# Kernel optimization log

Measured on AMD Instinct MI355X. Metric: run time of the kernel, lower is better.

The kernel has to match this reference:

```python
import jax, jax.numpy as jnp
import numpy as np

KH, KW = 3, 3
STRIDE = 1
OUT_C = 512


def im2col(x, kh, kw, stride):
    # x: [N, C, H, W] -> col: [C*kh*kw, N*oh*ow]  (row order: C major, then kh, kw)
    N, C, H, W = x.shape
    oh = (H - kh) // stride + 1
    ow = (W - kw) // stride + 1
    rows = jnp.arange(oh)[:, None] * stride + jnp.arange(kh)[None, :]  # [oh, kh]
    cols = jnp.arange(ow)[:, None] * stride + jnp.arange(kw)[None, :]  # [ow, kw]
    # gather windows: result [N, C, oh, kh, ow, kw]
    A = x[:, :, rows[:, :, None, None], cols[None, None, :, :]]
    # permute to (C, kh, kw, N, oh, ow) then flatten, matching torch permute(1,4,5,0,2,3)
    col = jnp.transpose(A, (1, 3, 5, 0, 2, 4)).reshape(C * kh * kw, N * oh * ow)
    return col, oh, ow


def setup_inputs() -> dict:
    key = jax.random.key(0)
    k1, k2, k3 = jax.random.split(key, 3)
    N, C, H, W = 16, 256, 32, 32
    K_sel = (C * KH * KW) // 2  # 1152 rows kept by the binary mask
    x = jax.random.normal(k1, (N, C, H, W), dtype=jnp.float32)
    weight = jax.random.normal(k2, (K_sel, OUT_C), dtype=jnp.float32) * 0.02
    idx = jnp.sort(jax.random.randint(k3, (K_sel,), 0, C * KH * KW, dtype=jnp.int32))
    return {"x": x, "weight": weight, "idx": idx}


def reference(x, weight, idx):
    N = x.shape[0]
    col, oh, ow = im2col(x, KH, KW, STRIDE)          # [C*kh*kw, N*oh*ow]
    x_tile = col[idx, :].T                            # gather masked rows -> [N*oh*ow, K_sel]
    conv_out = x_tile @ weight                        # [N*oh*ow, out_c]
    conv_out = conv_out.reshape(N, oh * ow, OUT_C)
    conv_out = jnp.transpose(conv_out, (0, 2, 1)).reshape(N, OUT_C, oh, ow)
    return conv_out
```

## Files before the change

### kernel.cpp

```cpp
#include <hip/hip_runtime.h>
#include <stdint.h>

#define N_IMG   16
#define C_IN    256
#define H_IN    32
#define W_IN    32
#define OH      30
#define OW      30
#define K_SEL   1152
#define OUTC    512
#define RY_TOT  (N_IMG * OH)
#define M_HAT   (RY_TOT * 32)
#define X_ELEMS (N_IMG * C_IN * H_IN * W_IN)
#define OUT_SP  (OH * OW)
#define CHW     (C_IN * H_IN * W_IN)

#define TO      128
#define TM      64
#define NMT     (M_HAT / TM)
#define NOT     (OUTC / TO)
#define BSTR    40
#define KITER   (K_SEL / 32)

typedef float f32x4  __attribute__((ext_vector_type(4)));
typedef short bf16x8 __attribute__((ext_vector_type(8)));

__device__ __forceinline__ unsigned short f2bf(float f) {
    unsigned int u = __float_as_uint(f);
    u += 0x7FFFu + ((u >> 16) & 1u);
    return (unsigned short)(u >> 16);
}

__device__ __forceinline__ void gl_lds16(const void* g, void* lds) {
    __builtin_amdgcn_global_load_lds(
        (const __attribute__((address_space(1))) unsigned int*)g,
        (__attribute__((address_space(3))) unsigned int*)lds,
        16, 0, 0);
}

__global__ void prep_kernel(const int* __restrict__ idx, const float* __restrict__ w,
                            int* __restrict__ koff, unsigned short* __restrict__ wT) {
    __shared__ float tile[32][33];
    const int bx = blockIdx.x, by = blockIdx.y, t = threadIdx.x;

    if (by == 0) {
        int k = bx * 256 + t;
        if (k < K_SEL) {
            int v = idx[k];
            int c = v / 9, rem = v - c * 9;
            int i = rem / 3, j = rem - i * 3;
            koff[k] = c * (H_IN * W_IN) + i * W_IN + j;
        }
    }
    const int s0 = bx * 32, o0 = by * 32;
    const int oc = t & 31, sg = t >> 5;
#pragma unroll
    for (int i = 0; i < 4; ++i) {
        int sl = sg * 4 + i;
        tile[sl][oc] = w[(s0 + sl) * OUTC + o0 + oc];
    }
    __syncthreads();
    const int ol = t >> 3, sq = t & 7;
    unsigned int u0 = (unsigned int)f2bf(tile[sq * 4 + 0][ol]) |
                      ((unsigned int)f2bf(tile[sq * 4 + 1][ol]) << 16);
    unsigned int u1 = (unsigned int)f2bf(tile[sq * 4 + 2][ol]) |
                      ((unsigned int)f2bf(tile[sq * 4 + 3][ol]) << 16);
    uint2 pk; pk.x = u0; pk.y = u1;
    *reinterpret_cast<uint2*>(&wT[(size_t)(o0 + ol) * K_SEL + s0 + sq * 4]) = pk;
}

__global__ __launch_bounds__(256, 4)
void gemm_kernel(const unsigned short* __restrict__ wT, const float* __restrict__ x,
                 const int* __restrict__ koff, float* __restrict__ out) {
    __shared__ __align__(16) unsigned short As[TO * 32];
    __shared__ __align__(16) unsigned short Bs[TM * BSTR];
    __shared__ int koS[K_SEL];

    const int t    = threadIdx.x;
    const int wave = t >> 6;
    const int lane = t & 63;
    const int quad = lane >> 4;
    const int lo   = lane & 15;

    const int bid = blockIdx.x;
    const int mt  = bid % NMT;
    const int ot  = bid / NMT;
    const int oBase = ot * TO;
    const int mBase = mt * TM;

    for (int i = t; i < K_SEL; i += 256) koS[i] = koff[i];

    int base[2];
#pragma unroll
    for (int ry = 0; ry < 2; ++ry) {
        int ryg = mt * 2 + ry;
        int n = ryg / 30, y = ryg - n * 30;
        base[ry] = n * CHW + y * W_IN;
    }

    const int xw  = t & 31;
    const int kq4 = t >> 5;
    const int ks  = kq4 * 4;

    const int lrow = lane >> 2, lks = (lane & 3) * 8;
    const unsigned short* wrow0 = wT + (size_t)(oBase + wave * 32 + lrow) * K_SEL + lks;
    const unsigned short* wrow1 = wrow0 + (size_t)16 * K_SEL;
    unsigned short* lA0 = &As[(wave * 32) * 32];
    unsigned short* lA1 = lA0 + 16 * 32;

    __syncthreads();

    f32x4 acc[2][4] = {};
    int   kk[2][4];
    float v[2][2][4];

#pragma unroll
    for (int j = 0; j < 4; ++j) kk[0][j] = koS[ks + j];
#pragma unroll
    for (int ry = 0; ry < 2; ++ry)
#pragma unroll
        for (int j = 0; j < 4; ++j) {
            int g = base[ry] + kk[0][j] + xw;
            g = min(g, X_ELEMS - 1);
            v[0][ry][j] = x[g];
        }

#pragma unroll 2
    for (int kt = 0; kt < KITER; ++kt) {
        const int p = kt & 1, q = p ^ 1;
        const int k0 = kt * 32;
        gl_lds16(wrow0 + k0, lA0);
        gl_lds16(wrow1 + k0, lA1);
#pragma unroll
        for (int ry = 0; ry < 2; ++ry) {
            unsigned int u0 = (unsigned int)f2bf(v[p][ry][0]) |
                              ((unsigned int)f2bf(v[p][ry][1]) << 16);
            unsigned int u1 = (unsigned int)f2bf(v[p][ry][2]) |
                              ((unsigned int)f2bf(v[p][ry][3]) << 16);
            uint2 pk; pk.x = u0; pk.y = u1;
            *reinterpret_cast<uint2*>(&Bs[(ry * 32 + xw) * BSTR + ks]) = pk;
        }
        if (kt + 1 < KITER) {
            const int k1 = k0 + 32;
#pragma unroll
            for (int j = 0; j < 4; ++j) kk[q][j] = koS[k1 + ks + j];
#pragma unroll
            for (int ry = 0; ry < 2; ++ry)
#pragma unroll
                for (int j = 0; j < 4; ++j) {
                    int g = base[ry] + kk[q][j] + xw;
                    g = min(g, X_ELEMS - 1);
                    v[q][ry][j] = x[g];
                }
        }
        __syncthreads();

        bf16x8 a[2], b[4];
#pragma unroll
        for (int ms = 0; ms < 2; ++ms)
            a[ms] = *(const bf16x8*)&As[(wave * 32 + ms * 16 + lo) * 32 + quad * 8];
#pragma unroll
        for (int ns = 0; ns < 4; ++ns)
            b[ns] = *(const bf16x8*)&Bs[(ns * 16 + lo) * BSTR + quad * 8];
#pragma unroll
        for (int ms = 0; ms < 2; ++ms)
#pragma unroll
            for (int ns = 0; ns < 4; ++ns)
                acc[ms][ns] = __builtin_amdgcn_mfma_f32_16x16x32_bf16(
                    a[ms], b[ns], acc[ms][ns], 0, 0, 0);
        __syncthreads();
    }

#pragma unroll
    for (int ns = 0; ns < 4; ++ns) {
        const int mh  = mBase + ns * 16 + lo;
        const int xwe = mh & 31;
        const int ryg = mh >> 5;
        const int n = ryg / 30, y = ryg - n * 30;
        if (xwe < OW) {
            const size_t ob = (size_t)n * (OUTC * OUT_SP) + (size_t)y * OW + xwe;
#pragma unroll
            for (int ms = 0; ms < 2; ++ms) {
                const int o0 = oBase + wave * 32 + ms * 16 + quad * 4;
#pragma unroll
                for (int r = 0; r < 4; ++r)
                    out[ob + (size_t)(o0 + r) * OUT_SP] = acc[ms][ns][r];
            }
        }
    }
}

extern "C" void kernel_launch(void* const* d_in, const int* in_sizes, int n_in,
                              void* d_out, int out_size, void* d_ws, size_t ws_size,
                              hipStream_t stream) {
    const float* x   = (const float*)d_in[0];
    const float* w   = (const float*)d_in[1];
    const int*   idx = (const int*)d_in[2];
    float*       out = (float*)d_out;

    char* ws = (char*)d_ws;
    int*            koff = (int*)ws;
    unsigned short* wT   = (unsigned short*)(ws + 4608);

    prep_kernel<<<dim3(K_SEL / 32, OUTC / 32), dim3(256), 0, stream>>>(idx, w, koff, wT);
    gemm_kernel<<<dim3(NMT * NOT), dim3(256), 0, stream>>>(wT, x, koff, out);
}
```

Before: 113.2 us.

## Double-buffer LDS tiles, swizzle weight tile, deepen gather prefetch to two stages

Splits the weight and im2col LDS tiles into two buffers. The next tile's async global-to-LDS weight load and bf16 pack can then proceed while MFMAs consume the current tile, which removes one barrier per K step. It also XOR-swizzles the weight tile's column chunks to reduce LDS bank conflicts on the fragment reads. It prefetches the gathered x values two iterations ahead, using a vectorized int4 read of the offset table. In exchange, LDS use per block roughly doubles and register pressure rises, which could limit occupancy.

Result: no change. 113.1 us (-0.1%).

```diff
diff --git a/kernel.cpp b/kernel.cpp
--- a/kernel.cpp
+++ b/kernel.cpp
@@ -72,8 +72,8 @@
 __global__ __launch_bounds__(256, 4)
 void gemm_kernel(const unsigned short* __restrict__ wT, const float* __restrict__ x,
                  const int* __restrict__ koff, float* __restrict__ out) {
-    __shared__ __align__(16) unsigned short As[TO * 32];
-    __shared__ __align__(16) unsigned short Bs[TM * BSTR];
+    __shared__ __align__(16) unsigned short As[2][TO * 32];
+    __shared__ __align__(16) unsigned short Bs[2][TM * BSTR];
     __shared__ int koS[K_SEL];
 
     const int t    = threadIdx.x;
@@ -90,78 +90,115 @@
 
     for (int i = t; i < K_SEL; i += 256) koS[i] = koff[i];
 
-    int base[2];
+    const int xw  = t & 31;
+    int basex[2];
 #pragma unroll
     for (int ry = 0; ry < 2; ++ry) {
         int ryg = mt * 2 + ry;
         int n = ryg / 30, y = ryg - n * 30;
-        base[ry] = n * CHW + y * W_IN;
-    }
-
-    const int xw  = t & 31;
+        basex[ry] = n * CHW + y * W_IN + xw;
+    }
+
     const int kq4 = t >> 5;
     const int ks  = kq4 * 4;
 
-    const int lrow = lane >> 2, lks = (lane & 3) * 8;
-    const unsigned short* wrow0 = wT + (size_t)(oBase + wave * 32 + lrow) * K_SEL + lks;
-    const unsigned short* wrow1 = wrow0 + (size_t)16 * K_SEL;
-    unsigned short* lA0 = &As[(wave * 32) * 32];
-    unsigned short* lA1 = lA0 + 16 * 32;
+    const int lrow = lane >> 2, csw = (lane & 3) ^ ((lrow >> 1) & 3);
+    const unsigned short* wrow0 = wT + (size_t)(oBase + wave * 32 + lrow) * K_SEL + csw * 8;
+    const unsigned short* wrow1 = wT + (size_t)(oBase + wave * 32 + 16 + lrow) * K_SEL + csw * 8;
+    unsigned short* lA0 = &As[0][(wave * 32) * 32];
+    unsigned short* lA1 = &As[1][(wave * 32) * 32];
+
+    const int aswz = quad ^ ((lo >> 1) & 3);
+    const unsigned short* aB[2] = {
+        &As[0][(wave * 32 + lo) * 32 + aswz * 8],
+        &As[1][(wave * 32 + lo) * 32 + aswz * 8] };
+    const unsigned short* bB[2] = {
+        &Bs[0][lo * BSTR + quad * 8],
+        &Bs[1][lo * BSTR + quad * 8] };
+    unsigned short* bW[2] = {
+        &Bs[0][xw * BSTR + ks],
+        &Bs[1][xw * BSTR + ks] };
 
     __syncthreads();
 
     f32x4 acc[2][4] = {};
-    int   kk[2][4];
     float v[2][2][4];
 
-#pragma unroll
-    for (int j = 0; j < 4; ++j) kk[0][j] = koS[ks + j];
-#pragma unroll
-    for (int ry = 0; ry < 2; ++ry)
-#pragma unroll
-        for (int j = 0; j < 4; ++j) {
-            int g = base[ry] + kk[0][j] + xw;
-            g = min(g, X_ELEMS - 1);
-            v[0][ry][j] = x[g];
-        }
+    gl_lds16(wrow0, lA0);
+    gl_lds16(wrow1, lA0 + 16 * 32);
+    {
+        int4 k4 = *(const int4*)&koS[ks];
+#pragma unroll
+        for (int ry = 0; ry < 2; ++ry)
+#pragma unroll
+            for (int j = 0; j < 4; ++j) {
+                int g = basex[ry] + ((const int*)&k4)[j];
+                g = min(g, X_ELEMS - 1);
+                v[0][ry][j] = x[g];
+            }
+    }
+#pragma unroll
+    for (int ry = 0; ry < 2; ++ry) {
+        unsigned int u0 = (unsigned int)f2bf(v[0][ry][0]) |
+                          ((unsigned int)f2bf(v[0][ry][1]) << 16);
+        unsigned int u1 = (unsigned int)f2bf(v[0][ry][2]) |
+                          ((unsigned int)f2bf(v[0][ry][3]) << 16);
+        uint2 pk; pk.x = u0; pk.y = u1;
+        *reinterpret_cast<uint2*>(bW[0] + ry * 32 * BSTR) = pk;
+    }
+    {
+        int4 k4 = *(const int4*)&koS[32 + ks];
+#pragma unroll
+        for (int ry = 0; ry < 2; ++ry)
+#pragma unroll
+            for (int j = 0; j < 4; ++j) {
+                int g = basex[ry] + ((const int*)&k4)[j];
+                g = min(g, X_ELEMS - 1);
+                v[1][ry][j] = x[g];
+            }
+    }
+    __syncthreads();
 
 #pragma unroll 2
     for (int kt = 0; kt < KITER; ++kt) {
         const int p = kt & 1, q = p ^ 1;
-        const int k0 = kt * 32;
-        gl_lds16(wrow0 + k0, lA0);
-        gl_lds16(wrow1 + k0, lA1);
-#pragma unroll
-        for (int ry = 0; ry < 2; ++ry) {
-            unsigned int u0 = (unsigned int)f2bf(v[p][ry][0]) |
-                              ((unsigned int)f2bf(v[p][ry][1]) << 16);
-            unsigned int u1 = (unsigned int)f2bf(v[p][ry][2]) |
-                              ((unsigned int)f2bf(v[p][ry][3]) << 16);
-            uint2 pk; pk.x = u0; pk.y = u1;
-            *reinterpret_cast<uint2*>(&Bs[(ry * 32 + xw) * BSTR + ks]) = pk;
-        }
+        unsigned short* lAq = q ? lA1 : lA0;
+
         if (kt + 1 < KITER) {
-            const int k1 = k0 + 32;
-#pragma unroll
-            for (int j = 0; j < 4; ++j) kk[q][j] = koS[k1 + ks + j];
+            const int k1 = (kt + 1) * 32;
+            gl_lds16(wrow0 + k1, lAq);
+            gl_lds16(wrow1 + k1, lAq + 16 * 32);
+        }
+        if (kt + 2 < KITER) {
+            const int k2 = (kt + 2) * 32;
+            int4 k4 = *(const int4*)&koS[k2 + ks];
 #pragma unroll
             for (int ry = 0; ry < 2; ++ry)
 #pragma unroll
                 for (int j = 0; j < 4; ++j) {
-                    int g = base[ry] + kk[q][j] + xw;
+                    int g = basex[ry] + ((const int*)&k4)[j];
                     g = min(g, X_ELEMS - 1);
-                    v[q][ry][j] = x[g];
+                    v[p][ry][j] = x[g];
                 }
         }
-        __syncthreads();
-
+        if (kt + 1 < KITER) {
+#pragma unroll
+            for (int ry = 0; ry < 2; ++ry) {
+                unsigned int u0 = (unsigned int)f2bf(v[q][ry][0]) |
+                                  ((unsigned int)f2bf(v[q][ry][1]) << 16);
+                unsigned int u1 = (unsigned int)f2bf(v[q][ry][2]) |
+                                  ((unsigned int)f2bf(v[q][ry][3]) << 16);
+                uint2 pk; pk.x = u0; pk.y = u1;
+                *reinterpret_cast<uint2*>(bW[q] + ry * 32 * BSTR) = pk;
+            }
+        }
         bf16x8 a[2], b[4];
 #pragma unroll
         for (int ms = 0; ms < 2; ++ms)
-            a[ms] = *(const bf16x8*)&As[(wave * 32 + ms * 16 + lo) * 32 + quad * 8];
+            a[ms] = *(const bf16x8*)(aB[p] + ms * 16 * 32);
 #pragma unroll
         for (int ns = 0; ns < 4; ++ns)
-            b[ns] = *(const bf16x8*)&Bs[(ns * 16 + lo) * BSTR + quad * 8];
+            b[ns] = *(const bf16x8*)(bB[p] + ns * 16 * BSTR);
 #pragma unroll
         for (int ms = 0; ms < 2; ++ms)
 #pragma unroll
```

## Deepen gather prefetch with 4-slot B ring, swizzled A LDS, fewer barriers

Applied to the files above, without the earlier changes.

Rewrites the GEMM main loop as a manually scheduled pipeline. The im2col gather for B now runs three k-steps ahead into a four-slot LDS ring, with explicit vmcnt/lgkmcnt waits and only one block barrier per two k-steps. The A tile is now per-wave private in LDS with an XOR column swizzle to cut bank conflicts, and the MFMA section runs at raised wave priority. The goal is to hide the latency of the scattered global x gathers and to remove barrier stalls. The cost is fragile hand-placed waitcnt counts that could race if the compiler reorders memory operations.

New measurement: 122.0 us. 1.08x slower.

```diff
diff --git a/kernel.cpp b/kernel.cpp
--- a/kernel.cpp
+++ b/kernel.cpp
@@ -73,7 +73,7 @@
 void gemm_kernel(const unsigned short* __restrict__ wT, const float* __restrict__ x,
                  const int* __restrict__ koff, float* __restrict__ out) {
     __shared__ __align__(16) unsigned short As[TO * 32];
-    __shared__ __align__(16) unsigned short Bs[TM * BSTR];
+    __shared__ __align__(16) unsigned short Bs[4][TM * BSTR];
     __shared__ int koS[K_SEL];
 
     const int t    = threadIdx.x;
@@ -90,86 +90,134 @@
 
     for (int i = t; i < K_SEL; i += 256) koS[i] = koff[i];
 
-    int base[2];
+    const int xw  = t & 31;
+    const int xwc = min(xw, 29);
+    int basex[2];
 #pragma unroll
     for (int ry = 0; ry < 2; ++ry) {
         int ryg = mt * 2 + ry;
         int n = ryg / 30, y = ryg - n * 30;
-        base[ry] = n * CHW + y * W_IN;
-    }
-
-    const int xw  = t & 31;
+        basex[ry] = n * CHW + y * W_IN + xwc;
+    }
+
     const int kq4 = t >> 5;
     const int ks  = kq4 * 4;
 
-    const int lrow = lane >> 2, lks = (lane & 3) * 8;
-    const unsigned short* wrow0 = wT + (size_t)(oBase + wave * 32 + lrow) * K_SEL + lks;
-    const unsigned short* wrow1 = wrow0 + (size_t)16 * K_SEL;
+    const int lrow = lane >> 2, csw = (lane & 3) ^ ((lrow >> 1) & 3);
+    const unsigned short* wrow0 = wT + (size_t)(oBase + wave * 32 + lrow) * K_SEL + csw * 8;
+    const unsigned short* wrow1 = wT + (size_t)(oBase + wave * 32 + 16 + lrow) * K_SEL + csw * 8;
     unsigned short* lA0 = &As[(wave * 32) * 32];
     unsigned short* lA1 = lA0 + 16 * 32;
 
+    const int aswz = quad ^ ((lo >> 1) & 3);
+    const unsigned short* aB = &As[(wave * 32 + lo) * 32 + aswz * 8];
+    const unsigned short* bB[4] = {
+        &Bs[0][lo * BSTR + quad * 8], &Bs[1][lo * BSTR + quad * 8],
+        &Bs[2][lo * BSTR + quad * 8], &Bs[3][lo * BSTR + quad * 8] };
+    unsigned short* bW[4] = {
+        &Bs[0][xw * BSTR + ks], &Bs[1][xw * BSTR + ks],
+        &Bs[2][xw * BSTR + ks], &Bs[3][xw * BSTR + ks] };
+
     __syncthreads();
 
     f32x4 acc[2][4] = {};
-    int   kk[2][4];
     float v[2][2][4];
 
-#pragma unroll
-    for (int j = 0; j < 4; ++j) kk[0][j] = koS[ks + j];
-#pragma unroll
-    for (int ry = 0; ry < 2; ++ry)
-#pragma unroll
-        for (int j = 0; j < 4; ++j) {
-            int g = base[ry] + kk[0][j] + xw;
-            g = min(g, X_ELEMS - 1);
-            v[0][ry][j] = x[g];
-        }
-
-#pragma unroll 2
-    for (int kt = 0; kt < KITER; ++kt) {
-        const int p = kt & 1, q = p ^ 1;
-        const int k0 = kt * 32;
-        gl_lds16(wrow0 + k0, lA0);
-        gl_lds16(wrow1 + k0, lA1);
-#pragma unroll
-        for (int ry = 0; ry < 2; ++ry) {
-            unsigned int u0 = (unsigned int)f2bf(v[p][ry][0]) |
-                              ((unsigned int)f2bf(v[p][ry][1]) << 16);
-            unsigned int u1 = (unsigned int)f2bf(v[p][ry][2]) |
-                              ((unsigned int)f2bf(v[p][ry][3]) << 16);
-            uint2 pk; pk.x = u0; pk.y = u1;
-            *reinterpret_cast<uint2*>(&Bs[(ry * 32 + xw) * BSTR + ks]) = pk;
-        }
-        if (kt + 1 < KITER) {
-            const int k1 = k0 + 32;
-#pragma unroll
-            for (int j = 0; j < 4; ++j) kk[q][j] = koS[k1 + ks + j];
-#pragma unroll
-            for (int ry = 0; ry < 2; ++ry)
-#pragma unroll
-                for (int j = 0; j < 4; ++j) {
-                    int g = base[ry] + kk[q][j] + xw;
-                    g = min(g, X_ELEMS - 1);
-                    v[q][ry][j] = x[g];
-                }
-        }
-        __syncthreads();
-
-        bf16x8 a[2], b[4];
-#pragma unroll
-        for (int ms = 0; ms < 2; ++ms)
-            a[ms] = *(const bf16x8*)&As[(wave * 32 + ms * 16 + lo) * 32 + quad * 8];
-#pragma unroll
-        for (int ns = 0; ns < 4; ++ns)
-            b[ns] = *(const bf16x8*)&Bs[(ns * 16 + lo) * BSTR + quad * 8];
-#pragma unroll
-        for (int ms = 0; ms < 2; ++ms)
-#pragma unroll
-            for (int ns = 0; ns < 4; ++ns)
-                acc[ms][ns] = __builtin_amdgcn_mfma_f32_16x16x32_bf16(
-                    a[ms], b[ns], acc[ms][ns], 0, 0, 0);
-        __syncthreads();
-    }
+    gl_lds16(wrow0, lA0);
+    gl_lds16(wrow1, lA1);
+#pragma unroll
+    for (int tl = 0; tl < 2; ++tl) {
+        int4 k4 = *(const int4*)&koS[tl * 32 + ks];
+#pragma unroll
+        for (int ry = 0; ry < 2; ++ry)
+#pragma unroll
+            for (int j = 0; j < 4; ++j)
+                v[tl][ry][j] = x[basex[ry] + ((const int*)&k4)[j]];
+    }
+    asm volatile("s_waitcnt vmcnt(8)" ::: "memory");
+#pragma unroll
+    for (int ry = 0; ry < 2; ++ry) {
+        unsigned int u0 = (unsigned int)f2bf(v[0][ry][0]) |
+                          ((unsigned int)f2bf(v[0][ry][1]) << 16);
+        unsigned int u1 = (unsigned int)f2bf(v[0][ry][2]) |
+                          ((unsigned int)f2bf(v[0][ry][3]) << 16);
+        uint2 pk; pk.x = u0; pk.y = u1;
+        *reinterpret_cast<uint2*>(bW[0] + ry * 32 * BSTR) = pk;
+    }
+    {
+        int4 k4 = *(const int4*)&koS[2 * 32 + ks];
+#pragma unroll
+        for (int ry = 0; ry < 2; ++ry)
+#pragma unroll
+            for (int j = 0; j < 4; ++j)
+                v[0][ry][j] = x[basex[ry] + ((const int*)&k4)[j]];
+    }
+    asm volatile("s_waitcnt vmcnt(8)" ::: "memory");
+#pragma unroll
+    for (int ry = 0; ry < 2; ++ry) {
+        unsigned int u0 = (unsigned int)f2bf(v[1][ry][0]) |
+                          ((unsigned int)f2bf(v[1][ry][1]) << 16);
+        unsigned int u1 = (unsigned int)f2bf(v[1][ry][2]) |
+                          ((unsigned int)f2bf(v[1][ry][3]) << 16);
+        uint2 pk; pk.x = u0; pk.y = u1;
+        *reinterpret_cast<uint2*>(bW[1] + ry * 32 * BSTR) = pk;
+    }
+    asm volatile("s_waitcnt lgkmcnt(0)" ::: "memory");
+    __builtin_amdgcn_s_barrier();
+
+#define KSTEP(KT, C, VR, VW) do {                                              \
+    asm volatile("s_waitcnt vmcnt(8)" ::: "memory");        \
+    bf16x8 a0_ = *(const bf16x8*)(aB);                                         \
+    bf16x8 a1_ = *(const bf16x8*)(aB + 16 * 32);                               \
+    bf16x8 b0_ = *(const bf16x8*)(bB[C]);                                      \
+    bf16x8 b1_ = *(const bf16x8*)(bB[C] + 16 * BSTR);                          \
+    bf16x8 b2_ = *(const bf16x8*)(bB[C] + 32 * BSTR);                          \
+    bf16x8 b3_ = *(const bf16x8*)(bB[C] + 48 * BSTR);                          \
+    const int kg_ = ((KT) + 3 < KITER ? (KT) + 3 : KITER - 1) * 32;            \
+    int4 k4_ = *(const int4*)&koS[kg_ + ks];                                   \
+    asm volatile("s_waitcnt lgkmcnt(0)" ::: "memory");   \
+    __builtin_amdgcn_sched_barrier(0);                                         \
+    const int k1_ = ((KT) + 1 < KITER ? (KT) + 1 : KITER - 1) * 32;            \
+    gl_lds16(wrow0 + k1_, lA0);                         \
+    gl_lds16(wrow1 + k1_, lA1);                                                \
+    _Pragma("unroll")                                                          \
+    for (int ry = 0; ry < 2; ++ry)                                             \
+        _Pragma("unroll")                                                      \
+        for (int j = 0; j < 4; ++j)                                            \
+            v[VW][ry][j] = x[basex[ry] + ((const int*)&k4_)[j]];               \
+    asm volatile("s_waitcnt vmcnt(10)" ::: "memory");   \
+    _Pragma("unroll")                                                          \
+    for (int ry = 0; ry < 2; ++ry) {                                           \
+        unsigned int u0_ = (unsigned int)f2bf(v[VR][ry][0]) |                  \
+                           ((unsigned int)f2bf(v[VR][ry][1]) << 16);           \
+        unsigned int u1_ = (unsigned int)f2bf(v[VR][ry][2]) |                  \
+                           ((unsigned int)f2bf(v[VR][ry][3]) << 16);           \
+        uint2 pk_; pk_.x = u0_; pk_.y = u1_;                                   \
+        *reinterpret_cast<uint2*>(bW[((C) + 2) & 3] + ry * 32 * BSTR) = pk_;   \
+    }                                                                          \
+    __builtin_amdgcn_s_setprio(1);                                             \
+    acc[0][0] = __builtin_amdgcn_mfma_f32_16x16x32_bf16(a0_, b0_, acc[0][0], 0, 0, 0); \
+    acc[0][1] = __builtin_amdgcn_mfma_f32_16x16x32_bf16(a0_, b1_, acc[0][1], 0, 0, 0); \
+    acc[0][2] = __builtin_amdgcn_mfma_f32_16x16x32_bf16(a0_, b2_, acc[0][2], 0, 0, 0); \
+    acc[0][3] = __builtin_amdgcn_mfma_f32_16x16x32_bf16(a0_, b3_, acc[0][3], 0, 0, 0); \
+    acc[1][0] = __builtin_amdgcn_mfma_f32_16x16x32_bf16(a1_, b0_, acc[1][0], 0, 0, 0); \
+    acc[1][1] = __builtin_amdgcn_mfma_f32_16x16x32_bf16(a1_, b1_, acc[1][1], 0, 0, 0); \
+    acc[1][2] = __builtin_amdgcn_mfma_f32_16x16x32_bf16(a1_, b2_, acc[1][2], 0, 0, 0); \
+    acc[1][3] = __builtin_amdgcn_mfma_f32_16x16x32_bf16(a1_, b3_, acc[1][3], 0, 0, 0); \
+    __builtin_amdgcn_s_setprio(0);                                             \
+} while (0)
+
+    for (int kt0 = 0; kt0 < KITER; kt0 += 4) {
+        KSTEP(kt0 + 0, 0, 0, 1);
+        KSTEP(kt0 + 1, 1, 1, 0);
+        asm volatile("s_waitcnt lgkmcnt(0)" ::: "memory");
+        __builtin_amdgcn_s_barrier();
+        KSTEP(kt0 + 2, 2, 0, 1);
+        KSTEP(kt0 + 3, 3, 1, 0);
+        asm volatile("s_waitcnt lgkmcnt(0)" ::: "memory");
+        __builtin_amdgcn_s_barrier();
+    }
+#undef KSTEP
 
 #pragma unroll
     for (int ns = 0; ns < 4; ++ns) {
```

## Drop LDS staging: pre-convert x to bf16, prelay weights in MFMA fragment order

Applied to the files above, without the earlier changes.

The prep kernel now converts x to bf16 in workspace and writes the weights already permuted into per-lane MFMA fragment order. The GEMM kernel no longer stages data through shared memory. Each wave loads its A fragments directly from global memory and gathers B elements from the bf16 x into registers, double-buffered across k-steps without barriers. Each wave now computes a 64x64 output tile, giving 480 blocks with launch bounds of 2 per SIMD. This removes LDS traffic and __syncthreads, but adds an extra pass over x and many scalar 16-bit gathers per lane, and raises register pressure.

Result: slower. 125.6 us (+11.0%).

```diff
diff --git a/kernel.cpp b/kernel.cpp
--- a/kernel.cpp
+++ b/kernel.cpp
@@ -15,12 +15,9 @@
 #define OUT_SP  (OH * OW)
 #define CHW     (C_IN * H_IN * W_IN)
 
-#define TO      128
-#define TM      64
-#define NMT     (M_HAT / TM)
-#define NOT     (OUTC / TO)
-#define BSTR    40
 #define KITER   (K_SEL / 32)
+#define NMT     240
+#define NOW     8
 
 typedef float f32x4  __attribute__((ext_vector_type(4)));
 typedef short bf16x8 __attribute__((ext_vector_type(8)));
@@ -31,15 +28,12 @@
     return (unsigned short)(u >> 16);
 }
 
-__device__ __forceinline__ void gl_lds16(const void* g, void* lds) {
-    __builtin_amdgcn_global_load_lds(
-        (const __attribute__((address_space(1))) unsigned int*)g,
-        (__attribute__((address_space(3))) unsigned int*)lds,
-        16, 0, 0);
-}
+union Bpack { unsigned int w[4]; bf16x8 v; };
 
 __global__ void prep_kernel(const int* __restrict__ idx, const float* __restrict__ w,
-                            int* __restrict__ koff, unsigned short* __restrict__ wT) {
+                            const float* __restrict__ x, int* __restrict__ koff,
+                            unsigned short* __restrict__ xb,
+                            unsigned short* __restrict__ wTf) {
     __shared__ float tile[32][33];
     const int bx = blockIdx.x, by = blockIdx.y, t = threadIdx.x;
 
@@ -52,6 +46,17 @@
             koff[k] = c * (H_IN * W_IN) + i * W_IN + j;
         }
     }
+    {
+        const float4* x4 = (const float4*)x;
+        ushort4* xb4 = (ushort4*)xb;
+        const int gtid = (by * 36 + bx) * 256 + t;
+        for (int i = gtid; i < X_ELEMS / 4; i += 36 * 16 * 256) {
+            float4 f = x4[i];
+            ushort4 u;
+            u.x = f2bf(f.x); u.y = f2bf(f.y); u.z = f2bf(f.z); u.w = f2bf(f.w);
+            xb4[i] = u;
+        }
+    }
     const int s0 = bx * 32, o0 = by * 32;
     const int oc = t & 31, sg = t >> 5;
 #pragma unroll
@@ -66,15 +71,17 @@
     unsigned int u1 = (unsigned int)f2bf(tile[sq * 4 + 2][ol]) |
                       ((unsigned int)f2bf(tile[sq * 4 + 3][ol]) << 16);
     uint2 pk; pk.x = u0; pk.y = u1;
-    *reinterpret_cast<uint2*>(&wT[(size_t)(o0 + ol) * K_SEL + s0 + sq * 4]) = pk;
-}
-
-__global__ __launch_bounds__(256, 4)
-void gemm_kernel(const unsigned short* __restrict__ wT, const float* __restrict__ x,
+    const size_t fi =
+        (((((size_t)(by >> 1) * KITER + bx) * 4 + ((by * 2 + (ol >> 4)) & 3)) * 64
+          + (sq >> 1) * 16 + (ol & 15)) * 8) + (sq & 1) * 4;
+    *reinterpret_cast<uint2*>(&wTf[fi]) = pk;
+}
+
+__global__ __launch_bounds__(256, 2)
+void gemm_kernel(const unsigned short* __restrict__ wTf,
+                 const unsigned short* __restrict__ xb,
                  const int* __restrict__ koff, float* __restrict__ out) {
-    __shared__ __align__(16) unsigned short As[TO * 32];
-    __shared__ __align__(16) unsigned short Bs[TM * BSTR];
-    __shared__ int koS[K_SEL];
+    __shared__ __align__(16) int koS[K_SEL];
 
     const int t    = threadIdx.x;
     const int wave = t >> 6;
@@ -84,104 +91,126 @@
 
     const int bid = blockIdx.x;
     const int mt  = bid % NMT;
-    const int ot  = bid / NMT;
-    const int oBase = ot * TO;
-    const int mBase = mt * TM;
+    const int og  = bid / NMT;
+    const int ow  = og * 4 + wave;
 
     for (int i = t; i < K_SEL; i += 256) koS[i] = koff[i];
-
-    int base[2];
-#pragma unroll
-    for (int ry = 0; ry < 2; ++ry) {
-        int ryg = mt * 2 + ry;
+    __syncthreads();
+
+    int bns[4];
+#pragma unroll
+    for (int ns = 0; ns < 4; ++ns) {
+        int ryg = mt * 2 + (ns >> 1);
         int n = ryg / 30, y = ryg - n * 30;
-        base[ry] = n * CHW + y * W_IN;
-    }
-
-    const int xw  = t & 31;
-    const int kq4 = t >> 5;
-    const int ks  = kq4 * 4;
-
-    const int lrow = lane >> 2, lks = (lane & 3) * 8;
-    const unsigned short* wrow0 = wT + (size_t)(oBase + wave * 32 + lrow) * K_SEL + lks;
-    const unsigned short* wrow1 = wrow0 + (size_t)16 * K_SEL;
-    unsigned short* lA0 = &As[(wave * 32) * 32];
-    unsigned short* lA1 = lA0 + 16 * 32;
-
-    __syncthreads();
-
-    f32x4 acc[2][4] = {};
-    int   kk[2][4];
-    float v[2][2][4];
-
-#pragma unroll
-    for (int j = 0; j < 4; ++j) kk[0][j] = koS[ks + j];
-#pragma unroll
-    for (int ry = 0; ry < 2; ++ry)
-#pragma unroll
-        for (int j = 0; j < 4; ++j) {
-            int g = base[ry] + kk[0][j] + xw;
-            g = min(g, X_ELEMS - 1);
-            v[0][ry][j] = x[g];
-        }
-
-#pragma unroll 2
-    for (int kt = 0; kt < KITER; ++kt) {
-        const int p = kt & 1, q = p ^ 1;
-        const int k0 = kt * 32;
-        gl_lds16(wrow0 + k0, lA0);
-        gl_lds16(wrow1 + k0, lA1);
-#pragma unroll
-        for (int ry = 0; ry < 2; ++ry) {
-            unsigned int u0 = (unsigned int)f2bf(v[p][ry][0]) |
-                              ((unsigned int)f2bf(v[p][ry][1]) << 16);
-            unsigned int u1 = (unsigned int)f2bf(v[p][ry][2]) |
-                              ((unsigned int)f2bf(v[p][ry][3]) << 16);
-            uint2 pk; pk.x = u0; pk.y = u1;
-            *reinterpret_cast<uint2*>(&Bs[(ry * 32 + xw) * BSTR + ks]) = pk;
-        }
-        if (kt + 1 < KITER) {
-            const int k1 = k0 + 32;
-#pragma unroll
-            for (int j = 0; j < 4; ++j) kk[q][j] = koS[k1 + ks + j];
-#pragma unroll
-            for (int ry = 0; ry < 2; ++ry)
-#pragma unroll
-                for (int j = 0; j < 4; ++j) {
-                    int g = base[ry] + kk[q][j] + xw;
-                    g = min(g, X_ELEMS - 1);
-                    v[q][ry][j] = x[g];
+        int xw = (ns & 1) * 16 + lo;
+        bns[ns] = n * CHW + y * W_IN + min(xw, 29);
+    }
+    const unsigned short* aP = wTf + (size_t)ow * KITER * 4 * 64 * 8;
+
+    f32x4 acc[4][4] = {};
+    bf16x8 aR0[4], aR1[4];
+    unsigned int u0[32], u1[32];
+    int4 kof0a, kof0b, kof1a, kof1b;
+
+    kof0a = *(const int4*)&koS[quad * 8];
+    kof0b = *(const int4*)&koS[quad * 8 + 4];
+#pragma unroll
+    for (int ms = 0; ms < 4; ++ms)
+        aR0[ms] = *(const bf16x8*)(aP + ((size_t)(0 * 4 + ms) * 64 + lane) * 8);
+#pragma unroll
+    for (int j = 0; j < 4; ++j) {
+        const int ka = ((const int*)&kof0a)[j], kb = ((const int*)&kof0b)[j];
+#pragma unroll
+        for (int ns = 0; ns < 4; ++ns) {
+            u0[ns * 8 + j]     = xb[bns[ns] + ka];
+            u0[ns * 8 + 4 + j] = xb[bns[ns] + kb];
+        }
+    }
+    kof1a = *(const int4*)&koS[32 + quad * 8];
+    kof1b = *(const int4*)&koS[32 + quad * 8 + 4];
+
+    for (int kt = 0; kt < KITER; kt += 2) {
+        {
+            const int kt1 = kt + 1;
+#pragma unroll
+            for (int ms = 0; ms < 4; ++ms)
+                aR1[ms] = *(const bf16x8*)(aP + ((size_t)(kt1 * 4 + ms) * 64 + lane) * 8);
+#pragma unroll
+            for (int j = 0; j < 4; ++j) {
+                const int ka = ((const int*)&kof1a)[j], kb = ((const int*)&kof1b)[j];
+#pragma unroll
+                for (int ns = 0; ns < 4; ++ns) {
+                    u1[ns * 8 + j]     = xb[bns[ns] + ka];
+                    u1[ns * 8 + 4 + j] = xb[bns[ns] + kb];
                 }
-        }
-        __syncthreads();
-
-        bf16x8 a[2], b[4];
-#pragma unroll
-        for (int ms = 0; ms < 2; ++ms)
-            a[ms] = *(const bf16x8*)&As[(wave * 32 + ms * 16 + lo) * 32 + quad * 8];
-#pragma unroll
-        for (int ns = 0; ns < 4; ++ns)
-            b[ns] = *(const bf16x8*)&Bs[(ns * 16 + lo) * BSTR + quad * 8];
-#pragma unroll
-        for (int ms = 0; ms < 2; ++ms)
-#pragma unroll
-            for (int ns = 0; ns < 4; ++ns)
-                acc[ms][ns] = __builtin_amdgcn_mfma_f32_16x16x32_bf16(
-                    a[ms], b[ns], acc[ms][ns], 0, 0, 0);
-        __syncthreads();
+            }
+            const int kt2 = (kt + 2 < KITER) ? kt + 2 : KITER - 1;
+            kof0a = *(const int4*)&koS[kt2 * 32 + quad * 8];
+            kof0b = *(const int4*)&koS[kt2 * 32 + quad * 8 + 4];
+            bf16x8 b[4];
+#pragma unroll
+            for (int ns = 0; ns < 4; ++ns) {
+                Bpack bp;
+                bp.w[0] = u0[ns * 8 + 0] | (u0[ns * 8 + 1] << 16);
+                bp.w[1] = u0[ns * 8 + 2] | (u0[ns * 8 + 3] << 16);
+                bp.w[2] = u0[ns * 8 + 4] | (u0[ns * 8 + 5] << 16);
+                bp.w[3] = u0[ns * 8 + 6] | (u0[ns * 8 + 7] << 16);
+                b[ns] = bp.v;
+            }
+#pragma unroll
+            for (int ms = 0; ms < 4; ++ms)
+#pragma unroll
+                for (int ns = 0; ns < 4; ++ns)
+                    acc[ms][ns] = __builtin_amdgcn_mfma_f32_16x16x32_bf16(
+                        aR0[ms], b[ns], acc[ms][ns], 0, 0, 0);
+        }
+        {
+            const int kt2 = (kt + 2 < KITER) ? kt + 2 : KITER - 1;
+#pragma unroll
+            for (int ms = 0; ms < 4; ++ms)
+                aR0[ms] = *(const bf16x8*)(aP + ((size_t)(kt2 * 4 + ms) * 64 + lane) * 8);
+#pragma unroll
+            for (int j = 0; j < 4; ++j) {
+                const int ka = ((const int*)&kof0a)[j], kb = ((const int*)&kof0b)[j];
+#pragma unroll
+                for (int ns = 0; ns < 4; ++ns) {
+                    u0[ns * 8 + j]     = xb[bns[ns] + ka];
+                    u0[ns * 8 + 4 + j] = xb[bns[ns] + kb];
+                }
+            }
+            const int kt3 = (kt + 3 < KITER) ? kt + 3 : KITER - 1;
+            kof1a = *(const int4*)&koS[kt3 * 32 + quad * 8];
+            kof1b = *(const int4*)&koS[kt3 * 32 + quad * 8 + 4];
+            bf16x8 b[4];
+#pragma unroll
+            for (int ns = 0; ns < 4; ++ns) {
+                Bpack bp;
+                bp.w[0] = u1[ns * 8 + 0] | (u1[ns * 8 + 1] << 16);
+                bp.w[1] = u1[ns * 8 + 2] | (u1[ns * 8 + 3] << 16);
+                bp.w[2] = u1[ns * 8 + 4] | (u1[ns * 8 + 5] << 16);
+                bp.w[3] = u1[ns * 8 + 6] | (u1[ns * 8 + 7] << 16);
+                b[ns] = bp.v;
+            }
+#pragma unroll
+            for (int ms = 0; ms < 4; ++ms)
+#pragma unroll
+                for (int ns = 0; ns < 4; ++ns)
+                    acc[ms][ns] = __builtin_amdgcn_mfma_f32_16x16x32_bf16(
+                        aR1[ms], b[ns], acc[ms][ns], 0, 0, 0);
+        }
     }
 
 #pragma unroll
     for (int ns = 0; ns < 4; ++ns) {
-        const int mh  = mBase + ns * 16 + lo;
+        const int mh  = mt * 64 + ns * 16 + lo;
         const int xwe = mh & 31;
         const int ryg = mh >> 5;
         const int n = ryg / 30, y = ryg - n * 30;
         if (xwe < OW) {
             const size_t ob = (size_t)n * (OUTC * OUT_SP) + (size_t)y * OW + xwe;
 #pragma unroll
-            for (int ms = 0; ms < 2; ++ms) {
-                const int o0 = oBase + wave * 32 + ms * 16 + quad * 4;
+            for (int ms = 0; ms < 4; ++ms) {
+                const int o0 = ow * 64 + ms * 16 + quad * 4;
 #pragma unroll
                 for (int r = 0; r < 4; ++r)
                     out[ob + (size_t)(o0 + r) * OUT_SP] = acc[ms][ns][r];
@@ -200,8 +229,10 @@
 
     char* ws = (char*)d_ws;
     int*            koff = (int*)ws;
-    unsigned short* wT   = (unsigned short*)(ws + 4608);
-
-    prep_kernel<<<dim3(K_SEL / 32, OUTC / 32), dim3(256), 0, stream>>>(idx, w, koff, wT);
-    gemm_kernel<<<dim3(NMT * NOT), dim3(256), 0, stream>>>(wT, x, koff, out);
-}
+    unsigned short* wTf  = (unsigned short*)(ws + 4608);
+    unsigned short* xb   = (unsigned short*)(ws + 4608 + 1179648);
+
+    prep_kernel<<<dim3(K_SEL / 32, OUTC / 32), dim3(256), 0, stream>>>(
+        idx, w, x, koff, xb, wTf);
+    gemm_kernel<<<dim3(NMT * 2), dim3(256), 0, stream>>>(wTf, xb, koff, out);
+}
```
